# Performance work log

Measured on AMD Instinct MI355X. Metric: run time of the kernel, lower is better.

## Reference

```python
import jax, jax.numpy as jnp
import numpy as np

JACCARD_THRESH = 0.5
NEGPOS_RATIO = 3
VAR = (0.1, 0.2)


def point_form(p):
    # center-size (cx,cy,w,h) -> corner (xmin,ymin,xmax,ymax)
    return jnp.concatenate([p[:, :2] - p[:, 2:] / 2, p[:, :2] + p[:, 2:] / 2], axis=1)


def jaccard(a, b):
    # a: [No,4] corner boxes, b: [Np,4] corner boxes -> IoU [No,Np]
    lt = jnp.maximum(a[:, None, :2], b[None, :, :2])
    rb = jnp.minimum(a[:, None, 2:], b[None, :, 2:])
    wh = jnp.clip(rb - lt, 0.0)
    inter = wh[..., 0] * wh[..., 1]
    area_a = ((a[:, 2] - a[:, 0]) * (a[:, 3] - a[:, 1]))[:, None]
    area_b = ((b[:, 2] - b[:, 0]) * (b[:, 3] - b[:, 1]))[None, :]
    return inter / (area_a + area_b - inter)


def encode(matched, priors):
    # matched: [Np,4] corner GT, priors: [Np,4] center-size
    g_cxcy = ((matched[:, :2] + matched[:, 2:]) / 2 - priors[:, :2]) / (VAR[0] * priors[:, 2:])
    g_wh = jnp.log((matched[:, 2:] - matched[:, :2]) / priors[:, 2:]) / VAR[1]
    return jnp.concatenate([g_cxcy, g_wh], axis=1)


def match_one(truths, labels, priors):
    # truths: [No,4], labels: [No], priors: [Np,4] center-size
    overlaps = jaccard(truths, point_form(priors))          # [No,Np]
    best_prior_idx = jnp.argmax(overlaps, axis=1)           # [No]
    best_truth_overlap = jnp.max(overlaps, axis=0)          # [Np]
    best_truth_idx = jnp.argmax(overlaps, axis=0)           # [Np]
    # each GT keeps its best prior (overlap forced to 2)
    best_truth_overlap = best_truth_overlap.at[best_prior_idx].set(2.0)
    best_truth_idx = best_truth_idx.at[best_prior_idx].set(jnp.arange(truths.shape[0]))
    matched = truths[best_truth_idx]                        # [Np,4]
    conf = labels[best_truth_idx].astype(jnp.int32) + 1     # background = 0
    conf = jnp.where(best_truth_overlap < JACCARD_THRESH, 0, conf)
    return encode(matched, priors), conf


def reference(loc_data, conf_data, dbox_list, targets):
    num_batch, num_dbox, num_classes = conf_data.shape
    truths = targets[:, :, :4]
    labels = targets[:, :, 4]
    loc_t, conf_t = jax.vmap(match_one, in_axes=(0, 0, None))(truths, labels, dbox_list)
    pos_mask = conf_t > 0                                   # [B,Np]
    # localization loss: SmoothL1 (beta=1), summed over positive dboxes
    diff = loc_data - loc_t
    ad = jnp.abs(diff)
    sl1 = jnp.where(ad < 1.0, 0.5 * diff * diff, ad - 0.5)
    loss_l = jnp.sum(sl1 * pos_mask[..., None].astype(sl1.dtype))
    # per-dbox cross entropy
    logp = jax.nn.log_softmax(conf_data, axis=-1)
    ce = -jnp.take_along_axis(logp, conf_t[..., None], axis=-1)[..., 0]  # [B,Np]
    # hard negative mining: rank (descending) of pos-zeroed CE via double argsort
    loss_c_hnm = jnp.where(pos_mask, 0.0, ce)
    loss_idx = jnp.argsort(-loss_c_hnm, axis=1)
    idx_rank = jnp.argsort(loss_idx, axis=1)
    num_pos = jnp.sum(pos_mask, axis=1, keepdims=True)      # [B,1]
    num_neg = jnp.minimum(num_pos * NEGPOS_RATIO, num_dbox)
    neg_mask = idx_rank < num_neg
    sel = jnp.logical_or(pos_mask, neg_mask)
    loss_c = jnp.sum(jnp.where(sel, ce, 0.0))
    N = jnp.sum(num_pos).astype(loss_l.dtype)
    return loss_l / N, loss_c / N


def setup_inputs() -> dict:
    key = jax.random.key(0)
    ks = jax.random.split(key, 7)
    B, Np, C, No = 128, 8732, 21, 16
    loc_data = jax.random.normal(ks[0], (B, Np, 4), dtype=jnp.float32) * 0.1
    conf_data = jax.random.normal(ks[1], (B, Np, C), dtype=jnp.float32)
    # default boxes in center-size form, w/h strictly positive
    cxcy = jax.random.uniform(ks[2], (Np, 2), minval=0.05, maxval=0.95)
    wh = jax.random.uniform(ks[3], (Np, 2), minval=0.05, maxval=0.5)
    dbox_list = jnp.concatenate([cxcy, wh], axis=1).astype(jnp.float32)
    # ground truth: valid corner-form boxes + class label in [0,20)
    gcxcy = jax.random.uniform(ks[4], (B, No, 2), minval=0.2, maxval=0.8)
    gwh = jax.random.uniform(ks[5], (B, No, 2), minval=0.05, maxval=0.3)
    boxes = jnp.concatenate([gcxcy - gwh / 2, gcxcy + gwh / 2], axis=-1)
    lab = jax.random.randint(ks[6], (B, No, 1), 0, C - 1).astype(jnp.float32)
    targets = jnp.concatenate([boxes, lab], axis=-1).astype(jnp.float32)
    return {"loc_data": loc_data, "conf_data": conf_data, "dbox_list": dbox_list, "targets": targets}
```

## Files before the change

kernel.cpp:

```cpp
#include <hip/hip_runtime.h>
#include <stdint.h>

#define TPB 256
#define SELTPB 1024
#define SELWAVES (SELTPB / 64)
#define MAXNO 64
#define NMB 16

__device__ __forceinline__ float sl1f(float d) {
    float ad = fabsf(d);
    return ad < 1.0f ? 0.5f * d * d : ad - 0.5f;
}

__device__ __forceinline__ float iou_pair(float tx1, float ty1, float tx2, float ty2, float ta,
                                          float px1, float py1, float px2, float py2, float pa) {
    float ltx = fmaxf(tx1, px1), lty = fmaxf(ty1, py1);
    float rbx = fminf(tx2, px2), rby = fminf(ty2, py2);
    float wx = fmaxf(rbx - ltx, 0.0f), wy = fmaxf(rby - lty, 0.0f);
    float inter = wx * wy;
    return inter / ((ta + pa) - inter);
}

template <int NO>
__global__ __launch_bounds__(256) void match_partial_kernel(
    const float* __restrict__ dbox, const float* __restrict__ targets,
    unsigned long long* __restrict__ pkeys, int Np, int No) {
    int b = blockIdx.y, mb = blockIdx.x;
    int tid = threadIdx.x;
    __shared__ float s_t[NO][5];
    __shared__ unsigned long long s_k[4][NO];
    if (tid < No) {
        const float* tr = targets + ((size_t)b * No + tid) * 5;
        float x1 = tr[0], y1 = tr[1], x2 = tr[2], y2 = tr[3];
        s_t[tid][0] = x1; s_t[tid][1] = y1; s_t[tid][2] = x2; s_t[tid][3] = y2;
        s_t[tid][4] = (x2 - x1) * (y2 - y1);
    }
    __syncthreads();
    int clen = (Np + NMB - 1) / NMB;
    int start = mb * clen;
    int end = start + clen;
    if (end > Np) end = Np;
    unsigned long long key[NO];
#pragma unroll
    for (int t = 0; t < NO; ++t) key[t] = 0ull;
    for (int p = start + tid; p < end; p += 256) {
        float4 pr = *reinterpret_cast<const float4*>(dbox + (size_t)p * 4);
        float px1 = pr.x - pr.z * 0.5f, py1 = pr.y - pr.w * 0.5f;
        float px2 = pr.x + pr.z * 0.5f, py2 = pr.y + pr.w * 0.5f;
        float pa = (px2 - px1) * (py2 - py1);
        unsigned lowp = 0xFFFFFFFFu - (unsigned)p;
#pragma unroll
        for (int t = 0; t < NO; ++t) {
            float iou = iou_pair(s_t[t][0], s_t[t][1], s_t[t][2], s_t[t][3], s_t[t][4],
                                 px1, py1, px2, py2, pa);
            unsigned long long k =
                (((unsigned long long)__float_as_uint(iou)) << 32) | (unsigned long long)lowp;
            if (k > key[t]) key[t] = k;
        }
    }
    int lane = tid & 63, wv = tid >> 6;
#pragma unroll
    for (int t = 0; t < NO; ++t) {
        unsigned long long k = key[t];
        for (int off = 32; off; off >>= 1) {
            unsigned long long o = __shfl_down(k, off);
            if (o > k) k = o;
        }
        if (lane == 0) s_k[wv][t] = k;
    }
    __syncthreads();
    if (tid < No) {
        unsigned long long m = s_k[0][tid];
#pragma unroll
        for (int w = 1; w < 4; ++w)
            if (s_k[w][tid] > m) m = s_k[w][tid];
        pkeys[((size_t)b * NMB + mb) * No + tid] = m;
    }
}

__global__ __launch_bounds__(64) void combine_kernel(
    const unsigned long long* __restrict__ pkeys, const float* __restrict__ targets,
    float* __restrict__ tmeta, int No) {
    int b = blockIdx.x, t = threadIdx.x;
    if (t >= No) return;
    unsigned long long k = pkeys[((size_t)b * NMB + 0) * No + t];
    for (int m = 1; m < NMB; ++m) {
        unsigned long long kk = pkeys[((size_t)b * NMB + m) * No + t];
        if (kk > k) k = kk;
    }
    const float* tr = targets + ((size_t)b * No + t) * 5;
    float x1 = tr[0], y1 = tr[1], x2 = tr[2], y2 = tr[3];
    float* tm = tmeta + ((size_t)b * MAXNO + t) * 8;
    tm[0] = x1; tm[1] = y1; tm[2] = x2; tm[3] = y2;
    tm[4] = (x2 - x1) * (y2 - y1);
    tm[5] = tr[4];
    tm[6] = __uint_as_float(0xFFFFFFFFu - (unsigned)(k & 0xFFFFFFFFull));
    tm[7] = 0.0f;
}

template <int CC, int TNO>
__global__ __launch_bounds__(TPB) void main_kernel(
    const float* __restrict__ loc, const float* __restrict__ conf,
    const float* __restrict__ dbox, const float* __restrict__ tmeta,
    float* __restrict__ v, float* __restrict__ part_l, float* __restrict__ part_c,
    int* __restrict__ part_n, int Np, int C, int No, int nchunk) {
    extern __shared__ float s_conf[];
    __shared__ float s_tb[MAXNO][5];
    __shared__ float s_red1[4];
    __shared__ float s_red2[4];
    __shared__ int s_redi[4];
    int b = blockIdx.y, chunk = blockIdx.x, tid = threadIdx.x;
    int p = chunk * TPB + tid;
    bool valid = p < Np;
    if (tid < No) {
        const float* tm = tmeta + ((size_t)b * MAXNO + tid) * 8;
        s_tb[tid][0] = tm[0]; s_tb[tid][1] = tm[1];
        s_tb[tid][2] = tm[2]; s_tb[tid][3] = tm[3];
        s_tb[tid][4] = tm[5];
    }
    int pbase = chunk * TPB;
    int cnt = Np - pbase;
    if (cnt > TPB) cnt = TPB;
    const float* cbase = conf + ((size_t)b * Np + (size_t)pbase) * C;
    {
        int ntot = cnt * C;
        int nv4 = ntot >> 2;
        const float4* c4 = reinterpret_cast<const float4*>(cbase);
        float4* s4 = reinterpret_cast<float4*>(s_conf);
        for (int i = tid; i < nv4; i += TPB) s4[i] = c4[i];
        for (int i = (nv4 << 2) + tid; i < ntot; i += TPB) s_conf[i] = cbase[i];
    }
    __syncthreads();

    float lossl = 0.0f, posce = 0.0f;
    int npos = 0;
    if (valid) {
        float4 pr = *reinterpret_cast<const float4*>(dbox + (size_t)p * 4);
        float px1 = pr.x - pr.z * 0.5f, py1 = pr.y - pr.w * 0.5f;
        float px2 = pr.x + pr.z * 0.5f, py2 = pr.y + pr.w * 0.5f;
        float pa = (px2 - px1) * (py2 - py1);
        float bov = -1.0f;
        int bidx = 0;
        int ovt = -1;
        if (TNO > 0) {
#pragma unroll
            for (int t = 0; t < TNO; ++t) {
                const float* tm = tmeta + ((size_t)b * MAXNO + t) * 8;
                float iou = iou_pair(tm[0], tm[1], tm[2], tm[3], tm[4],
                                     px1, py1, px2, py2, pa);
                if (iou > bov) { bov = iou; bidx = t; }
                if (__float_as_uint(tm[6]) == (unsigned)p) ovt = t;
            }
        } else {
            for (int t = 0; t < No; ++t) {
                const float* tm = tmeta + ((size_t)b * MAXNO + t) * 8;
                float iou = iou_pair(tm[0], tm[1], tm[2], tm[3], tm[4],
                                     px1, py1, px2, py2, pa);
                if (iou > bov) { bov = iou; bidx = t; }
                if (__float_as_uint(tm[6]) == (unsigned)p) ovt = t;
            }
        }
        if (ovt >= 0) { bidx = ovt; bov = 2.0f; }
        int ct = (bov < 0.5f) ? 0 : ((int)s_tb[bidx][4] + 1);
        float ce;
        if (CC > 0) {
            const float* crow = s_conf + tid * CC;
            float fr[CC > 0 ? CC : 1];
            float mx = -1e30f, fc = 0.0f;
#pragma unroll
            for (int j = 0; j < CC; ++j) {
                float x = crow[j];
                fr[j] = x;
                mx = fmaxf(mx, x);
                fc = (j == ct) ? x : fc;
            }
            float s = 0.0f;
#pragma unroll
            for (int j = 0; j < CC; ++j) s += __expf(fr[j] - mx);
            ce = __logf(s) + mx - fc;
        } else {
            const float* crow = s_conf + (size_t)tid * C;
            float mx = crow[0];
            for (int j = 1; j < C; ++j) mx = fmaxf(mx, crow[j]);
            float s = 0.0f;
            for (int j = 0; j < C; ++j) s += __expf(crow[j] - mx);
            ce = __logf(s) + mx - crow[ct];
        }
        bool pos = ct > 0;
        v[(size_t)b * Np + p] = pos ? 0.0f : ce;
        if (pos) {
            posce = ce;
            npos = 1;
            float mx1 = s_tb[bidx][0], my1 = s_tb[bidx][1];
            float mx2 = s_tb[bidx][2], my2 = s_tb[bidx][3];
            float gcx = ((mx1 + mx2) * 0.5f - pr.x) / (0.1f * pr.z);
            float gcy = ((my1 + my2) * 0.5f - pr.y) / (0.1f * pr.w);
            float gw = __logf((mx2 - mx1) / pr.z) / 0.2f;
            float gh = __logf((my2 - my1) / pr.w) / 0.2f;
            float4 l4 = *reinterpret_cast<const float4*>(loc + ((size_t)b * Np + p) * 4);
            lossl = sl1f(l4.x - gcx) + sl1f(l4.y - gcy) + sl1f(l4.z - gw) + sl1f(l4.w - gh);
        }
    }
    float a1 = lossl, a2 = posce;
    int ni = npos;
    for (int off = 32; off; off >>= 1) {
        a1 += __shfl_down(a1, off);
        a2 += __shfl_down(a2, off);
        ni += __shfl_down(ni, off);
    }
    if ((tid & 63) == 0) {
        s_red1[tid >> 6] = a1;
        s_red2[tid >> 6] = a2;
        s_redi[tid >> 6] = ni;
    }
    __syncthreads();
    if (tid == 0) {
        part_l[(size_t)b * nchunk + chunk] = s_red1[0] + s_red1[1] + s_red1[2] + s_red1[3];
        part_c[(size_t)b * nchunk + chunk] = s_red2[0] + s_red2[1] + s_red2[2] + s_red2[3];
        part_n[(size_t)b * nchunk + chunk] = s_redi[0] + s_redi[1] + s_redi[2] + s_redi[3];
    }
}

__global__ __launch_bounds__(SELTPB) void select_kernel(
    const float* __restrict__ v, const float* __restrict__ pl,
    const float* __restrict__ pc, const int* __restrict__ pn,
    float* __restrict__ row_res, int Np, int nchunk, int negpos) {
    int b = blockIdx.x, tid = threadIdx.x;
    int lane = tid & 63, wv = tid >> 6;
    extern __shared__ unsigned sv[];
    __shared__ unsigned whist[SELWAVES][256];
    __shared__ unsigned suf[257];
    __shared__ float s_f[SELWAVES];
    __shared__ int s_dig, s_acc;
    __shared__ float s_lossl, s_posce;
    __shared__ int s_np;

    if (wv == 0) {
        float a = 0.0f, c = 0.0f;
        int n = 0;
        for (int i = lane; i < nchunk; i += 64) {
            a += pl[(size_t)b * nchunk + i];
            c += pc[(size_t)b * nchunk + i];
            n += pn[(size_t)b * nchunk + i];
        }
        for (int off = 32; off; off >>= 1) {
            a += __shfl_down(a, off);
            c += __shfl_down(c, off);
            n += __shfl_down(n, off);
        }
        if (lane == 0) { s_lossl = a; s_posce = c; s_np = n; }
    }
    {
        const float4* v4 = reinterpret_cast<const float4*>(v + (size_t)b * Np);
        int n4 = Np >> 2;
        for (int i = tid; i < n4; i += SELTPB) {
            float4 f = v4[i];
            uint4 u;
            u.x = __float_as_uint(f.x); u.y = __float_as_uint(f.y);
            u.z = __float_as_uint(f.z); u.w = __float_as_uint(f.w);
            *reinterpret_cast<uint4*>(&sv[i << 2]) = u;
        }
        for (int i = (n4 << 2) + tid; i < Np; i += SELTPB)
            sv[i] = __float_as_uint(v[(size_t)b * Np + i]);
    }
    __syncthreads();
    int npos = s_np;
    int K = npos * negpos;
    if (K > Np) K = Np;
    float lossc = s_posce;
    if (K > 0) {
        unsigned prefix = 0;
        int Krem = K;
        for (int shift = 24; shift >= 0; shift -= 8) {
            for (int i = tid; i < SELWAVES * 256; i += SELTPB)
                (&whist[0][0])[i] = 0;
            __syncthreads();
            for (int i = tid; i < Np; i += SELTPB) {
                unsigned u = sv[i];
                bool match = (shift == 24) || ((u >> (shift + 8)) == (prefix >> (shift + 8)));
                if (match) atomicAdd(&whist[wv][(u >> shift) & 0xFFu], 1u);
            }
            __syncthreads();
            if (tid < 256) {
                unsigned t = 0;
                for (int w = 0; w < SELWAVES; ++w) t += whist[w][tid];
                suf[tid] = t;
            }
            if (tid == 0) suf[256] = 0;
            __syncthreads();
            for (int off = 1; off < 256; off <<= 1) {
                unsigned add = 0;
                if (tid < 256 && tid + off < 256) add = suf[tid + off];
                __syncthreads();
                if (tid < 256) suf[tid] += add;
                __syncthreads();
            }
            if (tid < 256) {
                unsigned S = suf[tid];
                unsigned Snext = suf[tid + 1];
                if ((int)S >= Krem && (int)Snext < Krem) { s_dig = tid; s_acc = (int)Snext; }
            }
            __syncthreads();
            prefix |= ((unsigned)s_dig) << shift;
            Krem -= s_acc;
            __syncthreads();
        }
        float sum_gt = 0.0f;
        for (int i = tid; i < Np; i += SELTPB) {
            unsigned u = sv[i];
            if (u > prefix) sum_gt += __uint_as_float(u);
        }
        for (int off = 32; off; off >>= 1) sum_gt += __shfl_down(sum_gt, off);
        if (lane == 0) s_f[wv] = sum_gt;
        __syncthreads();
        if (tid == 0) {
            float t = 0.0f;
            for (int w = 0; w < SELWAVES; ++w) t += s_f[w];
            lossc += t + (float)Krem * __uint_as_float(prefix);
        }
    }
    if (tid == 0) {
        row_res[(size_t)b * 3 + 0] = s_lossl;
        row_res[(size_t)b * 3 + 1] = lossc;
        row_res[(size_t)b * 3 + 2] = (float)npos;
    }
}

__global__ __launch_bounds__(TPB) void finalize_kernel(
    const float* __restrict__ row_res, float* __restrict__ out, int B) {
    int tid = threadIdx.x;
    float l = 0, c = 0, n = 0;
    for (int i = tid; i < B; i += TPB) {
        l += row_res[(size_t)i * 3 + 0];
        c += row_res[(size_t)i * 3 + 1];
        n += row_res[(size_t)i * 3 + 2];
    }
    __shared__ float sl[4], sc[4], sn[4];
    for (int off = 32; off; off >>= 1) {
        l += __shfl_down(l, off);
        c += __shfl_down(c, off);
        n += __shfl_down(n, off);
    }
    int lane = tid & 63, w = tid >> 6;
    if (lane == 0) { sl[w] = l; sc[w] = c; sn[w] = n; }
    __syncthreads();
    if (tid == 0) {
        l = sl[0] + sl[1] + sl[2] + sl[3];
        c = sc[0] + sc[1] + sc[2] + sc[3];
        n = sn[0] + sn[1] + sn[2] + sn[3];
        out[0] = l / n;
        out[1] = c / n;
    }
}

extern "C" void kernel_launch(void* const* d_in, const int* in_sizes, int n_in,
                              void* d_out, int out_size, void* d_ws, size_t ws_size,
                              hipStream_t stream) {
    const float* loc = (const float*)d_in[0];
    const float* conf = (const float*)d_in[1];
    const float* dbox = (const float*)d_in[2];
    const float* targets = (const float*)d_in[3];

    int Np = in_sizes[2] / 4;
    int B = in_sizes[0] / (Np * 4);
    int C = in_sizes[1] / (B * Np);
    int No = in_sizes[3] / (B * 5);
    int nchunk = (Np + TPB - 1) / TPB;

    char* w = (char*)d_ws;
    unsigned long long* pkeys = (unsigned long long*)w;
    w += (size_t)B * NMB * No * sizeof(unsigned long long);
    float* tmeta = (float*)w;
    w += (size_t)B * MAXNO * 8 * sizeof(float);
    float* v = (float*)w;
    w += (size_t)B * Np * sizeof(float);
    float* part_l = (float*)w;
    w += (size_t)B * nchunk * sizeof(float);
    float* part_c = (float*)w;
    w += (size_t)B * nchunk * sizeof(float);
    int* part_n = (int*)w;
    w += (size_t)B * nchunk * sizeof(int);
    float* row_res = (float*)w;

    dim3 mgrid(NMB, B);
    if (No == 16)
        match_partial_kernel<16><<<mgrid, 256, 0, stream>>>(dbox, targets, pkeys, Np, No);
    else
        match_partial_kernel<MAXNO><<<mgrid, 256, 0, stream>>>(dbox, targets, pkeys, Np, No);

    combine_kernel<<<B, 64, 0, stream>>>(pkeys, targets, tmeta, No);

    dim3 grid(nchunk, B);
    size_t lds_main = (size_t)TPB * C * sizeof(float);
    if (C == 21 && No == 16)
        main_kernel<21, 16><<<grid, TPB, lds_main, stream>>>(loc, conf, dbox, tmeta,
                                                             v, part_l, part_c, part_n, Np, C, No, nchunk);
    else
        main_kernel<0, 0><<<grid, TPB, lds_main, stream>>>(loc, conf, dbox, tmeta,
                                                           v, part_l, part_c, part_n, Np, C, No, nchunk);
    select_kernel<<<B, SELTPB, (size_t)Np * sizeof(float), stream>>>(v, part_l, part_c, part_n,
                                                                     row_res, Np, nchunk, 3);
    finalize_kernel<<<1, TPB, 0, stream>>>(row_res, (float*)d_out, B);
}
```

Before: 89.04 us.

## Drop LDS conf staging, process 4 priors per thread, wave-level histogram scan

```diff
diff --git a/kernel.cpp b/kernel.cpp
--- a/kernel.cpp
+++ b/kernel.cpp
@@ -2,6 +2,7 @@
 #include <stdint.h>
 
 #define TPB 256
+#define PPT 4
 #define SELTPB 1024
 #define SELWAVES (SELTPB / 64)
 #define MAXNO 64
@@ -104,37 +105,26 @@
     const float* __restrict__ dbox, const float* __restrict__ tmeta,
     float* __restrict__ v, float* __restrict__ part_l, float* __restrict__ part_c,
     int* __restrict__ part_n, int Np, int C, int No, int nchunk) {
-    extern __shared__ float s_conf[];
     __shared__ float s_tb[MAXNO][5];
     __shared__ float s_red1[4];
     __shared__ float s_red2[4];
     __shared__ int s_redi[4];
     int b = blockIdx.y, chunk = blockIdx.x, tid = threadIdx.x;
-    int p = chunk * TPB + tid;
-    bool valid = p < Np;
+    int pbase = chunk * (TPB * PPT);
     if (tid < No) {
         const float* tm = tmeta + ((size_t)b * MAXNO + tid) * 8;
         s_tb[tid][0] = tm[0]; s_tb[tid][1] = tm[1];
         s_tb[tid][2] = tm[2]; s_tb[tid][3] = tm[3];
         s_tb[tid][4] = tm[5];
     }
-    int pbase = chunk * TPB;
-    int cnt = Np - pbase;
-    if (cnt > TPB) cnt = TPB;
-    const float* cbase = conf + ((size_t)b * Np + (size_t)pbase) * C;
-    {
-        int ntot = cnt * C;
-        int nv4 = ntot >> 2;
-        const float4* c4 = reinterpret_cast<const float4*>(cbase);
-        float4* s4 = reinterpret_cast<float4*>(s_conf);
-        for (int i = tid; i < nv4; i += TPB) s4[i] = c4[i];
-        for (int i = (nv4 << 2) + tid; i < ntot; i += TPB) s_conf[i] = cbase[i];
-    }
     __syncthreads();
 
     float lossl = 0.0f, posce = 0.0f;
     int npos = 0;
-    if (valid) {
+#pragma unroll 1
+    for (int pp = 0; pp < PPT; ++pp) {
+        int p = pbase + pp * TPB + tid;
+        if (p >= Np) break;
         float4 pr = *reinterpret_cast<const float4*>(dbox + (size_t)p * 4);
         float px1 = pr.x - pr.z * 0.5f, py1 = pr.y - pr.w * 0.5f;
         float px2 = pr.x + pr.z * 0.5f, py2 = pr.y + pr.w * 0.5f;
@@ -163,8 +153,8 @@
         if (ovt >= 0) { bidx = ovt; bov = 2.0f; }
         int ct = (bov < 0.5f) ? 0 : ((int)s_tb[bidx][4] + 1);
         float ce;
+        const float* crow = conf + ((size_t)b * Np + p) * C;
         if (CC > 0) {
-            const float* crow = s_conf + tid * CC;
             float fr[CC > 0 ? CC : 1];
             float mx = -1e30f, fc = 0.0f;
 #pragma unroll
@@ -179,7 +169,6 @@
             for (int j = 0; j < CC; ++j) s += __expf(fr[j] - mx);
             ce = __logf(s) + mx - fc;
         } else {
-            const float* crow = s_conf + (size_t)tid * C;
             float mx = crow[0];
             for (int j = 1; j < C; ++j) mx = fmaxf(mx, crow[j]);
             float s = 0.0f;
@@ -189,8 +178,8 @@
         bool pos = ct > 0;
         v[(size_t)b * Np + p] = pos ? 0.0f : ce;
         if (pos) {
-            posce = ce;
-            npos = 1;
+            posce += ce;
+            npos += 1;
             float mx1 = s_tb[bidx][0], my1 = s_tb[bidx][1];
             float mx2 = s_tb[bidx][2], my2 = s_tb[bidx][3];
             float gcx = ((mx1 + mx2) * 0.5f - pr.x) / (0.1f * pr.z);
@@ -198,7 +187,7 @@
             float gw = __logf((mx2 - mx1) / pr.z) / 0.2f;
             float gh = __logf((my2 - my1) / pr.w) / 0.2f;
             float4 l4 = *reinterpret_cast<const float4*>(loc + ((size_t)b * Np + p) * 4);
-            lossl = sl1f(l4.x - gcx) + sl1f(l4.y - gcy) + sl1f(l4.z - gw) + sl1f(l4.w - gh);
+            lossl += sl1f(l4.x - gcx) + sl1f(l4.y - gcy) + sl1f(l4.z - gw) + sl1f(l4.w - gh);
         }
     }
     float a1 = lossl, a2 = posce;
@@ -229,7 +218,6 @@
     int lane = tid & 63, wv = tid >> 6;
     extern __shared__ unsigned sv[];
     __shared__ unsigned whist[SELWAVES][256];
-    __shared__ unsigned suf[257];
     __shared__ float s_f[SELWAVES];
     __shared__ int s_dig, s_acc;
     __shared__ float s_lossl, s_posce;
@@ -281,29 +269,32 @@
                 if (match) atomicAdd(&whist[wv][(u >> shift) & 0xFFu], 1u);
             }
             __syncthreads();
-            if (tid < 256) {
-                unsigned t = 0;
-                for (int w = 0; w < SELWAVES; ++w) t += whist[w][tid];
-                suf[tid] = t;
-            }
-            if (tid == 0) suf[256] = 0;
-            __syncthreads();
-            for (int off = 1; off < 256; off <<= 1) {
-                unsigned add = 0;
-                if (tid < 256 && tid + off < 256) add = suf[tid + off];
-                __syncthreads();
-                if (tid < 256) suf[tid] += add;
-                __syncthreads();
-            }
-            if (tid < 256) {
-                unsigned S = suf[tid];
-                unsigned Snext = suf[tid + 1];
-                if ((int)S >= Krem && (int)Snext < Krem) { s_dig = tid; s_acc = (int)Snext; }
+            if (wv == 0) {
+                unsigned t0 = 0, t1 = 0, t2 = 0, t3 = 0;
+#pragma unroll
+                for (int w = 0; w < SELWAVES; ++w) {
+                    t0 += whist[w][4 * lane + 0];
+                    t1 += whist[w][4 * lane + 1];
+                    t2 += whist[w][4 * lane + 2];
+                    t3 += whist[w][4 * lane + 3];
+                }
+                unsigned s = t0 + t1 + t2 + t3;
+                unsigned run = s;
+                for (int off = 1; off < 64; off <<= 1) {
+                    unsigned o = __shfl_down(run, off);
+                    if (lane + off < 64) run += o;
+                }
+                unsigned hi = run - s;
+                unsigned S3 = hi + t3, S2 = S3 + t2, S1 = S2 + t1, S0 = S1 + t0;
+                unsigned kr = (unsigned)Krem;
+                if (S3 >= kr && hi < kr) { s_dig = 4 * lane + 3; s_acc = (int)hi; }
+                else if (S2 >= kr && S3 < kr) { s_dig = 4 * lane + 2; s_acc = (int)S3; }
+                else if (S1 >= kr && S2 < kr) { s_dig = 4 * lane + 1; s_acc = (int)S2; }
+                else if (S0 >= kr && S1 < kr) { s_dig = 4 * lane + 0; s_acc = (int)S1; }
             }
             __syncthreads();
             prefix |= ((unsigned)s_dig) << shift;
             Krem -= s_acc;
-            __syncthreads();
         }
         float sum_gt = 0.0f;
         for (int i = tid; i < Np; i += SELTPB) {
@@ -365,7 +356,7 @@
     int B = in_sizes[0] / (Np * 4);
     int C = in_sizes[1] / (B * Np);
     int No = in_sizes[3] / (B * 5);
-    int nchunk = (Np + TPB - 1) / TPB;
+    int nchunk = (Np + TPB * PPT - 1) / (TPB * PPT);
 
     char* w = (char*)d_ws;
     unsigned long long* pkeys = (unsigned long long*)w;
@@ -391,13 +382,12 @@
     combine_kernel<<<B, 64, 0, stream>>>(pkeys, targets, tmeta, No);
 
     dim3 grid(nchunk, B);
-    size_t lds_main = (size_t)TPB * C * sizeof(float);
     if (C == 21 && No == 16)
-        main_kernel<21, 16><<<grid, TPB, lds_main, stream>>>(loc, conf, dbox, tmeta,
-                                                             v, part_l, part_c, part_n, Np, C, No, nchunk);
+        main_kernel<21, 16><<<grid, TPB, 0, stream>>>(loc, conf, dbox, tmeta,
+                                                      v, part_l, part_c, part_n, Np, C, No, nchunk);
     else
-        main_kernel<0, 0><<<grid, TPB, lds_main, stream>>>(loc, conf, dbox, tmeta,
-                                                           v, part_l, part_c, part_n, Np, C, No, nchunk);
+        main_kernel<0, 0><<<grid, TPB, 0, stream>>>(loc, conf, dbox, tmeta,
+                                                    v, part_l, part_c, part_n, Np, C, No, nchunk);
     select_kernel<<<B, SELTPB, (size_t)Np * sizeof(float), stream>>>(v, part_l, part_c, part_n,
                                                                      row_res, Np, nchunk, 3);
     finalize_kernel<<<1, TPB, 0, stream>>>(row_res, (float*)d_out, B);
```

Result: faster. 84.24 us (-5.4%).
